# Kernel optimization log

Hardware: AMD Instinct MI355X
Metric: run time of the kernel (lower is better)

Reference implementation:

```python
import jax, jax.numpy as jnp
import numpy as np


def conv1d(x, w, b):
    # x: (N, Cin, W), w: (Cout, Cin, K) -> (N, Cout, W-K+1), VALID conv (torch Conv1d)
    y = jax.lax.conv_general_dilated(x, w, (1,), 'VALID', dimension_numbers=('NCH', 'OIH', 'NCH'))
    return y + b[None, :, None]


def cnn_block(x, w, b):
    # conv1d then MaxPool1d over the full valid length -> (N, Cout)
    return jnp.max(conv1d(x, w, b), axis=2)


def highway(x, Wp, bp, Wg, bg):
    p = jax.nn.relu(x @ Wp.T + bp)
    g = jax.nn.sigmoid(x @ Wg.T + bg)
    return g * p + (1.0 - g) * x


def lstm_masked(x, lens, Wih, Whh, bih, bhh):
    # x: (N, Wt, E); lens: (N,) valid lengths. Emulates pack_padded_sequence +
    # nn.LSTM + pad_packed_sequence: outputs are h_t for t < len, zeros after.
    N, Wt, _ = x.shape
    H = Whh.shape[1]
    bias = bih + bhh
    h0 = jnp.zeros((N, H), x.dtype)

    def step(carry, inp):
        xt, t = inp
        h, c = carry
        z = xt @ Wih.T + h @ Whh.T + bias  # (N, 4H), gate order i,f,g,o
        i, f, g, o = jnp.split(z, 4, axis=-1)
        c2 = jax.nn.sigmoid(f) * c + jax.nn.sigmoid(i) * jnp.tanh(g)
        h2 = jax.nn.sigmoid(o) * jnp.tanh(c2)
        valid = (t < lens)[:, None]
        h2 = jnp.where(valid, h2, h)
        c2 = jnp.where(valid, c2, c)
        return (h2, c2), jnp.where(valid, h2, jnp.zeros_like(h2))

    xs = jnp.moveaxis(x, 1, 0)  # (Wt, N, E)
    ts = jnp.arange(Wt)
    _, out = jax.lax.scan(step, (h0, h0), (xs, ts))
    return jnp.moveaxis(out, 0, 1)  # (N, Wt, H)


def setup_inputs() -> dict:
    key = jax.random.key(0)
    ks = jax.random.split(key, 32)
    B, T = 32, 48
    WL, WA, WE = 33, 50, 30
    EL, EA, EE, H = 300, 988, 20, 128
    CL, CA, CE = 128, 256, 64
    s = 0.02
    inp = {
        'x_lin': jax.random.normal(ks[0], (B, T, WL, EL), jnp.float32),
        'x_aco': jax.random.normal(ks[1], (B, T, WA, EA), jnp.float32),
        'x_emo': jax.random.normal(ks[2], (B, T, WE, EE), jnp.float32),
        'window_length': jax.random.randint(ks[3], (B, T), 0, WE).astype(jnp.int32) + 1,
        'length': jax.random.randint(ks[4], (B,), 1, T + 1).astype(jnp.int32),
        # CNN params
        'convL_w': s * jax.random.normal(ks[5], (CL, EL, 5), jnp.float32),
        'convL_b': jnp.zeros((CL,), jnp.float32),
        'convA_w': s * jax.random.normal(ks[6], (CA, EA, 10), jnp.float32),
        'convA_b': jnp.zeros((CA,), jnp.float32),
        'convE_w': s * jax.random.normal(ks[7], (CE, H, 3), jnp.float32),
        'convE_b': jnp.zeros((CE,), jnp.float32),
        # Highway params
        'hwL_Wp': s * jax.random.normal(ks[8], (CL, CL), jnp.float32),
        'hwL_bp': jnp.zeros((CL,), jnp.float32),
        'hwL_Wg': s * jax.random.normal(ks[9], (CL, CL), jnp.float32),
        'hwL_bg': jnp.zeros((CL,), jnp.float32),
        'hwA_Wp': s * jax.random.normal(ks[10], (CA, CA), jnp.float32),
        'hwA_bp': jnp.zeros((CA,), jnp.float32),
        'hwA_Wg': s * jax.random.normal(ks[11], (CA, CA), jnp.float32),
        'hwA_bg': jnp.zeros((CA,), jnp.float32),
        'hwE_Wp': s * jax.random.normal(ks[12], (CE, CE), jnp.float32),
        'hwE_bp': jnp.zeros((CE,), jnp.float32),
        'hwE_Wg': s * jax.random.normal(ks[13], (CE, CE), jnp.float32),
        'hwE_bg': jnp.zeros((CE,), jnp.float32),
        # LSTM params (nn.LSTM, 1 layer, batch_first)
        'lstm_Wih': s * jax.random.normal(ks[14], (4 * H, EE), jnp.float32),
        'lstm_Whh': s * jax.random.normal(ks[15], (4 * H, H), jnp.float32),
        'lstm_bih': jnp.zeros((4 * H,), jnp.float32),
        'lstm_bhh': jnp.zeros((4 * H,), jnp.float32),
    }
    return inp


def reference(x_lin, x_aco, x_emo, window_length, length,
              convL_w, convL_b, convA_w, convA_b, convE_w, convE_b,
              hwL_Wp, hwL_bp, hwL_Wg, hwL_bg,
              hwA_Wp, hwA_bp, hwA_Wg, hwA_bg,
              hwE_Wp, hwE_bp, hwE_Wg, hwE_bg,
              lstm_Wih, lstm_Whh, lstm_bih, lstm_bhh):
    B, T = x_lin.shape[:2]
    # Linguistic: per-window CNN + Highway (dropout = identity in eval)
    xl = x_lin.reshape(B * T, x_lin.shape[2], x_lin.shape[3]).transpose(0, 2, 1)  # (BT, 300, WL)
    outL = highway(cnn_block(xl, convL_w, convL_b), hwL_Wp, hwL_bp, hwL_Wg, hwL_bg)
    outL = outL.reshape(B, T, -1)
    # Acoustic
    xa = x_aco.reshape(B * T, x_aco.shape[2], x_aco.shape[3]).transpose(0, 2, 1)  # (BT, 988, WA)
    outA = highway(cnn_block(xa, convA_w, convA_b), hwA_Wp, hwA_bp, hwA_Wg, hwA_bg)
    outA = outA.reshape(B, T, -1)
    # Emotient: ragged per-window LSTM (packed semantics) -> CNN -> Highway
    xe = x_emo.reshape(B * T, x_emo.shape[2], x_emo.shape[3])  # (BT, WE, 20)
    lens = window_length.reshape(B * T)
    h = lstm_masked(xe, lens, lstm_Wih, lstm_Whh, lstm_bih, lstm_bhh)  # (BT, WE, 128)
    outE = highway(cnn_block(h.transpose(0, 2, 1), convE_w, convE_b), hwE_Wp, hwE_bp, hwE_Wg, hwE_bg)
    outE = outE.reshape(B, T, -1)
    # Concatenate modalities -> (B, T, 128+256+64) fed to the downstream head
    return jnp.concatenate([outL, outA, outE], axis=2)
```

## Files before the change

kernel.cpp:

```cpp
#include <hip/hip_runtime.h>
#include <hip/hip_bf16.h>
#include <math.h>

#define BTOT 1536
#define EL 300
#define ELP 304
#define WL_ 33
#define CL 128
#define LOUTL 29
#define KPL 1536
#define EA 988
#define EAP 992
#define WA_ 50
#define CA 256
#define LOUTA 41
#define KPA 9920
#define EE 20
#define WE_ 30
#define HH 128
#define CE 64
#define LOUTE 28
#define KPE 384
#define KDIML 1500
#define KDIMA 9880
#define KDIME 384

typedef __attribute__((ext_vector_type(4))) float f32x4;
typedef __attribute__((ext_vector_type(8))) short short8;

__device__ __forceinline__ unsigned short f2bf(float f) {
    unsigned int x = __float_as_uint(f);
    unsigned int r = (x + 0x7fffu + ((x >> 16) & 1u)) >> 16;
    return (unsigned short)r;
}

__device__ __forceinline__ float sigmf(float x) {
    return __builtin_amdgcn_rcpf(1.f + __expf(-x));
}
__device__ __forceinline__ float tanh_fast(float x) {
    return 1.f - 2.f * __builtin_amdgcn_rcpf(1.f + __expf(2.f * x));
}

#define GLD16(gp, lp) __builtin_amdgcn_global_load_lds( \
    (const __attribute__((address_space(1))) void*)(gp), \
    (__attribute__((address_space(3))) void*)(lp), 16, 0, 0)

template<int N> __device__ __forceinline__ void vmwait() {
    if constexpr (N == 0) asm volatile("s_waitcnt vmcnt(0)" ::: "memory");
    else if constexpr (N == 2) asm volatile("s_waitcnt vmcnt(2)" ::: "memory");
    else if constexpr (N == 3) asm volatile("s_waitcnt vmcnt(3)" ::: "memory");
    else static_assert(N == 0 || N == 2 || N == 3, "add case");
}

__device__ __forceinline__ void tr_one(const float* a, float* at, int R, int C, int idx) {
    int r = idx / C, c = idx - r * C;
    at[c * R + r] = a[idx];
}
template<int CIN, int CINP, int KW, int COUT, int KPAD>
__device__ __forceinline__ void wt_one(const float* w, unsigned short* wt, int idx) {
    int co = idx / KPAD;
    int p  = idx - co * KPAD;
    int k  = p / CINP;
    int c  = p - k * CINP;
    float v = 0.f;
    if (k < KW && c < CIN) v = w[(co * CIN + c) * KW + k];
    wt[idx] = f2bf(v);
}
template<bool BIG>
__global__ void prep_small(const float* hwL_Wp, float* WpTL, const float* hwL_Wg, float* WgTL,
                           const float* hwA_Wp, float* WpTA, const float* hwA_Wg, float* WgTA,
                           const float* hwE_Wp, float* WpTE, const float* hwE_Wg, float* WgTE,
                           const float* lstm_Wih, float* WihT, const float* lstm_Whh, float* WhhT,
                           const float* convL_w, unsigned short* wtL,
                           const float* convE_w, unsigned short* wtE,
                           unsigned short* whh_bf, unsigned short* wihp_bf) {
    constexpr int S1 = 16384, S2 = 16384, S3 = 65536, S4 = 65536, S5 = 4096, S6 = 4096;
    constexpr int S7 = 512 * 20, S8 = 512 * 128;
    constexpr int S9 = 128 * KPL, S10 = 64 * KPE, S11 = 512 * 128, S12 = 512 * 32;
    constexpr int SMALL = S1 + S2 + S3 + S4 + S5 + S6 + S7 + S8;
    constexpr int TOTAL = BIG ? (SMALL + S9 + S10 + S11 + S12) : SMALL;
    int stride = gridDim.x * blockDim.x;
    for (int i = blockIdx.x * blockDim.x + threadIdx.x; i < TOTAL; i += stride) {
        int idx = i;
        if (idx < S1) { tr_one(hwL_Wp, WpTL, 128, 128, idx); continue; } idx -= S1;
        if (idx < S2) { tr_one(hwL_Wg, WgTL, 128, 128, idx); continue; } idx -= S2;
        if (idx < S3) { tr_one(hwA_Wp, WpTA, 256, 256, idx); continue; } idx -= S3;
        if (idx < S4) { tr_one(hwA_Wg, WgTA, 256, 256, idx); continue; } idx -= S4;
        if (idx < S5) { tr_one(hwE_Wp, WpTE, 64, 64, idx); continue; } idx -= S5;
        if (idx < S6) { tr_one(hwE_Wg, WgTE, 64, 64, idx); continue; } idx -= S6;
        if (idx < S7) { tr_one(lstm_Wih, WihT, 512, 20, idx); continue; } idx -= S7;
        if (idx < S8) { tr_one(lstm_Whh, WhhT, 512, 128, idx); continue; } idx -= S8;
        if constexpr (BIG) {
            if (idx < S9) { wt_one<EL, ELP, 5, CL, KPL>(convL_w, wtL, idx); continue; } idx -= S9;
            if (idx < S10) { wt_one<HH, HH, 3, CE, KPE>(convE_w, wtE, idx); continue; } idx -= S10;
            if (idx < S11) { whh_bf[idx] = f2bf(lstm_Whh[idx]); continue; } idx -= S11;
            { int col = idx >> 5, e = idx & 31;
              wihp_bf[idx] = (e < 20) ? f2bf(lstm_Wih[col * 20 + e]) : (unsigned short)0; }
        }
    }
}

__global__ void prep_wtA(const float* __restrict__ w, unsigned short* __restrict__ wt) {
    int idx = blockIdx.x * blockDim.x + threadIdx.x;
    if (idx >= CA * KPA) return;
    wt_one<EA, EAP, 10, CA, KPA>(w, wt, idx);
}

template<int CIN, int CINP>
__device__ __forceinline__ void cvt_chunk(const float* in, unsigned short* out, int idx) {
    constexpr int CH = CINP / 8;
    int row = idx / CH, c0 = (idx - row * CH) * 8;
    const float* src = in + (size_t)row * CIN + c0;
    union { short8 s; unsigned short u[8]; } o;
    if (c0 + 8 <= CIN) {
        float4 v0 = *(const float4*)src;
        float4 v1 = *(const float4*)(src + 4);
        o.u[0]=f2bf(v0.x); o.u[1]=f2bf(v0.y); o.u[2]=f2bf(v0.z); o.u[3]=f2bf(v0.w);
        o.u[4]=f2bf(v1.x); o.u[5]=f2bf(v1.y); o.u[6]=f2bf(v1.z); o.u[7]=f2bf(v1.w);
    } else {
        #pragma unroll
        for (int j = 0; j < 8; ++j) o.u[j] = (c0 + j < CIN) ? f2bf(src[j]) : (unsigned short)0;
    }
    *(short8*)(out + (size_t)row * CINP + c0) = o.s;
}
__global__ void cvt_both(const float* __restrict__ xa, const float* __restrict__ xl,
                         unsigned short* __restrict__ outa, unsigned short* __restrict__ outl) {
    constexpr int NAC = (BTOT * WA_) * (EAP / 8);
    constexpr int NLC = (BTOT * WL_) * (ELP / 8);
    int stride = gridDim.x * blockDim.x;
    for (int i = blockIdx.x * blockDim.x + threadIdx.x; i < NAC + NLC; i += stride) {
        if (i < NAC) cvt_chunk<EA, EAP>(xa, outa, i);
        else         cvt_chunk<EL, ELP>(xl, outl, i - NAC);
    }
}

template<int NBT, int LOUT, int WIN, int CINP, int COUT, int KPAD>
__global__ __launch_bounds__(512, 4)
void conv_pool_v5(const unsigned short* __restrict__ xb, const unsigned short* __restrict__ wt,
                  const float* __restrict__ bias, float* __restrict__ pooled)
{
    constexpr int NF   = COUT / 64;
    constexpr int NK   = KPAD / 32;
    constexpr int NBU  = COUT / 16;
    constexpr int BWI  = (NBU > 8) ? NBU / 8 : 1;
    constexpr int VMN  = 1 + BWI;
    constexpr int ABY  = 128 * 64;
    constexpr int BUFB = ABY + COUT * 64;
    constexpr int MVAL = NBT * LOUT;

    __shared__ __align__(16) char smem[3 * BUFB > 32768 ? 3 * BUFB : 32768];

    const int tid  = threadIdx.x;
    const int lane = tid & 63;
    const int wid  = tid >> 6;
    const int wm   = wid >> 2;
    const int wn   = wid & 3;
    const int lr   = lane & 15;
    const int lq   = lane >> 4;
    const int bx   = blockIdx.x;

    f32x4 acc[4][NF];
    #pragma unroll
    for (int i = 0; i < 4; ++i)
        #pragma unroll
        for (int j = 0; j < NF; ++j) acc[i][j] = (f32x4){0.f, 0.f, 0.f, 0.f};

    const int sr   = wid * 16 + (lane >> 2);
    const int sslt = lane & 3;
    int rv = (sr < MVAL) ? sr : (MVAL - 1);
    int sbtl = rv / LOUT;
    int sl   = rv - sbtl * LOUT;
    const char* asrc0 = (const char*)xb + (((size_t)(bx * NBT + sbtl) * WIN + sl) * CINP) * 2
                      + ((sslt * 16) ^ (((sr >> 2) & 3) << 4));

    auto STAGE = [&](int ts, int buf) {
        char* db = smem + buf * BUFB;
        GLD16(asrc0 + (size_t)ts * 64, db + wid * 1024 + lane * 16);
        #pragma unroll
        for (int i = 0; i < BWI; ++i) {
            int bu = (NBU > 8) ? (wid + i * 8) : (wid & (NBU - 1));
            int col = bu * 16 + (lane >> 2);
            const char* src = (const char*)wt + (size_t)col * KPAD * 2
                + (size_t)ts * 64 + ((sslt * 16) ^ (((col >> 2) & 3) << 4));
            GLD16(src, db + ABY + bu * 1024 + lane * 16);
        }
    };

    STAGE(0, 0);
    STAGE(1, 1);
    vmwait<VMN>();
    __builtin_amdgcn_s_barrier();

    const int ra = wm * 64 + lr;
    int cur = 0;
    for (int t = 0; t < NK; ++t) {
        const char* sA = smem + cur * BUFB;
        const char* sB = sA + ABY;
        short8 a[4];
        #pragma unroll
        for (int o = 0; o < 4; ++o) {
            int r = ra + o * 16;
            a[o] = *(const short8*)(sA + (size_t)r * 64 + ((lq * 16) ^ (((r >> 2) & 3) << 4)));
        }
        short8 bfr[NF];
        #pragma unroll
        for (int nf = 0; nf < NF; ++nf) {
            int cb = wn * (16 * NF) + nf * 16 + lr;
            bfr[nf] = *(const short8*)(sB + (size_t)cb * 64 + ((lq * 16) ^ (((cb >> 2) & 3) << 4)));
        }
        int wb = cur + 2; if (wb >= 3) wb -= 3;
        if (t + 2 < NK) STAGE(t + 2, wb);
        asm volatile("s_waitcnt lgkmcnt(0)" ::: "memory");
        __builtin_amdgcn_sched_barrier(0);
        __builtin_amdgcn_s_setprio(1);
        #pragma unroll
        for (int nf = 0; nf < NF; ++nf)
            #pragma unroll
            for (int o = 0; o < 4; ++o)
                acc[o][nf] = __builtin_amdgcn_mfma_f32_16x16x32_bf16(a[o], bfr[nf], acc[o][nf], 0, 0, 0);
        __builtin_amdgcn_s_setprio(0);
        if (t + 2 < NK) vmwait<VMN>(); else vmwait<0>();
        asm volatile("" ::: "memory");
        __builtin_amdgcn_s_barrier();
        cur = cur + 1; if (cur >= 3) cur -= 3;
    }
    __syncthreads();

    for (int nf = 0; nf < NF; ++nf) {
        #pragma unroll
        for (int m = 0; m < 4; ++m) {
            int row = wm * 64 + m * 16 + lq * 4;
            int cs  = wn * 16 + lr;
            f32x4 v = acc[m][nf];
            #pragma unroll
            for (int r = 0; r < 4; ++r)
                *(float*)(smem + (size_t)(row + r) * 256 + ((cs * 4) ^ (((row + r) & 7) << 4))) = v[r];
        }
        __syncthreads();
        if (tid < 64 * NBT) {
            int btl = tid >> 6, cs = tid & 63;
            int base = btl * LOUT;
            float m = *(const float*)(smem + (size_t)base * 256 + ((cs * 4) ^ ((base & 7) << 4)));
            for (int l = 1; l < LOUT; ++l) {
                int rr = base + l;
                m = fmaxf(m, *(const float*)(smem + (size_t)rr * 256 + ((cs * 4) ^ ((rr & 7) << 4))));
            }
            int col = (cs >> 4) * (16 * NF) + nf * 16 + (cs & 15);
            int bt  = bx * NBT + btl;
            pooled[(size_t)bt * COUT + col] = m + bias[col];
        }
        __syncthreads();
    }
}

__global__ __launch_bounds__(512, 1)
void lstm_mfma(const float* __restrict__ x_emo,
               const unsigned short* __restrict__ wihp_bf, const unsigned short* __restrict__ whh_bf,
               const float* __restrict__ bih, const float* __restrict__ bhh,
               const int* __restrict__ lens, unsigned short* __restrict__ hbuf)
{
    __shared__ __align__(16) unsigned short xq[WE_ * 16 * 32];
    __shared__ __align__(16) char h_s[2 * 16 * HH * 2];

    const int tid  = threadIdx.x;
    const int w    = tid >> 6;
    const int lane = tid & 63;
    const int lr   = lane & 15;
    const int lq   = lane >> 4;
    const int s0   = blockIdx.x * 16;
    const int c    = w * 16 + lr;

    short8 bfr[4][4];
    short8 bw[4];
    float bj[4];
    #pragma unroll
    for (int g = 0; g < 4; ++g) {
        int col = g * 128 + c;
        #pragma unroll
        for (int kt = 0; kt < 4; ++kt)
            bfr[g][kt] = *(const short8*)(whh_bf + (size_t)col * 128 + kt * 32 + lq * 8);
        bw[g] = *(const short8*)(wihp_bf + (size_t)col * 32 + lq * 8);
        bj[g] = bih[col] + bhh[col];
    }
    int len4[4];
    #pragma unroll
    for (int j = 0; j < 4; ++j) len4[j] = lens[s0 + lq * 4 + j];

    for (int i = tid; i < WE_ * 16 * 32; i += 512) {
        int t = i >> 9, r = (i >> 5) & 15, e = i & 31;
        xq[i] = (e < 20) ? f2bf(x_emo[(((size_t)(s0 + r) * WE_) + t) * 20 + e]) : (unsigned short)0;
    }
    for (int i = tid; i < 2048; i += 512) ((unsigned int*)h_s)[i] = 0u;

    float c_prev[4] = {0.f, 0.f, 0.f, 0.f};
    unsigned short hb_prev[4] = {0, 0, 0, 0};
    __syncthreads();

    for (int t = 0; t < WE_; ++t) {
        const char* hsr = h_s + (t & 1) * 4096;
        char* hsw = h_s + ((t & 1) ^ 1) * 4096;
        short8 ax = *(const short8*)((const char*)xq + (size_t)(t * 16 + lr) * 64 + lq * 16);
        short8 af[4];
        #pragma unroll
        for (int kt = 0; kt < 4; ++kt)
            af[kt] = *(const short8*)(hsr + ((lr * 256 + kt * 64 + lq * 16) ^ ((lr & 7) << 4)));
        f32x4 acc[4];
        #pragma unroll
        for (int g = 0; g < 4; ++g)
            acc[g] = __builtin_amdgcn_mfma_f32_16x16x32_bf16(ax, bw[g], (f32x4){0.f,0.f,0.f,0.f}, 0, 0, 0);
        #pragma unroll
        for (int kt = 0; kt < 4; ++kt)
            #pragma unroll
            for (int g = 0; g < 4; ++g)
                acc[g] = __builtin_amdgcn_mfma_f32_16x16x32_bf16(af[kt], bfr[g][kt], acc[g], 0, 0, 0);
        #pragma unroll
        for (int j = 0; j < 4; ++j) {
            int s = lq * 4 + j;
            float zi = acc[0][j] + bj[0];
            float zf = acc[1][j] + bj[1];
            float zg = acc[2][j] + bj[2];
            float zo = acc[3][j] + bj[3];
            float si = sigmf(zi), sf = sigmf(zf), so = sigmf(zo);
            float tg = tanh_fast(zg);
            float c2 = sf * c_prev[j] + si * tg;
            float h2 = so * tanh_fast(c2);
            bool valid = (t < len4[j]);
            c_prev[j] = valid ? c2 : c_prev[j];
            unsigned short h2b = f2bf(h2);
            unsigned short hn = valid ? h2b : hb_prev[j];
            hb_prev[j] = hn;
            *(unsigned short*)(hsw + (((s * HH + c) * 2) ^ ((s & 7) << 4))) = hn;
            hbuf[(((size_t)(s0 + s) * WE_) + t) * HH + c] = valid ? h2b : (unsigned short)0;
        }
        __syncthreads();
    }
}

template<int C, int OFF>
__global__ void highway_kernel(const float* __restrict__ pooled,
                               const float* __restrict__ WpT, const float* __restrict__ bp,
                               const float* __restrict__ WgT, const float* __restrict__ bg,
                               float* __restrict__ out) {
    int bt = blockIdx.x;
    int j  = threadIdx.x;
    __shared__ float xs[C];
    xs[j] = pooled[(size_t)bt * C + j];
    __syncthreads();
    float ap = bp[j], ag = bg[j];
    for (int cc = 0; cc < C; ++cc) {
        float xv = xs[cc];
        ap += xv * WpT[cc * C + j];
        ag += xv * WgT[cc * C + j];
    }
    float p = fmaxf(ap, 0.f);
    float g = sigmf(ag);
    out[(size_t)bt * 448 + OFF + j] = g * p + (1.f - g) * xs[j];
}

__global__ __launch_bounds__(512)
void lstm_kernel_f32(const float* __restrict__ x, const int* __restrict__ lens,
                     const float* __restrict__ WihT, const float* __restrict__ WhhT,
                     const float* __restrict__ bih, const float* __restrict__ bhh,
                     float* __restrict__ hout) {
    int bt = blockIdx.x;
    int j  = threadIdx.x;
    __shared__ float xs[WE_][EE];
    __shared__ __align__(16) float hs[HH];
    __shared__ float zs[512];
    for (int idx = j; idx < WE_ * EE; idx += 512)
        ((float*)xs)[idx] = x[(size_t)bt * WE_ * EE + idx];
    if (j < HH) hs[j] = 0.f;
    float wih[EE];
    #pragma unroll
    for (int e = 0; e < EE; ++e) wih[e] = WihT[e * 512 + j];
    float whh[HH];
    #pragma unroll
    for (int h = 0; h < HH; ++h) whh[h] = WhhT[h * 512 + j];
    float bjv = bih[j] + bhh[j];
    float c_reg = 0.f;
    int len = lens[bt];
    __syncthreads();
    for (int t = 0; t < WE_; ++t) {
        float z = bjv;
        #pragma unroll
        for (int e = 0; e < EE; ++e) z += wih[e] * xs[t][e];
        const float4* h4 = (const float4*)hs;
        #pragma unroll
        for (int q = 0; q < HH / 4; ++q) {
            float4 hv = h4[q];
            z += whh[4*q+0] * hv.x + whh[4*q+1] * hv.y
               + whh[4*q+2] * hv.z + whh[4*q+3] * hv.w;
        }
        zs[j] = z;
        __syncthreads();
        if (j < HH) {
            float zi = zs[j], zf = zs[HH + j], zg = zs[2*HH + j], zo = zs[3*HH + j];
            float si = 1.f / (1.f + expf(-zi));
            float sf = 1.f / (1.f + expf(-zf));
            float so = 1.f / (1.f + expf(-zo));
            float tg = tanhf(zg);
            float c2 = sf * c_reg + si * tg;
            float h2 = so * tanhf(c2);
            bool valid = (t < len);
            float hn = valid ? h2 : hs[j];
            c_reg    = valid ? c2 : c_reg;
            hout[((size_t)bt * WE_ + t) * HH + j] = valid ? h2 : 0.f;
            hs[j] = hn;
        }
        __syncthreads();
    }
}

template<int CIN, int WIN, int COUT, int KDIM, int LOUT>
__global__ __launch_bounds__(256)
void conv_pool_simple(const float* __restrict__ x, const float* __restrict__ w,
                      const float* __restrict__ bias, float* __restrict__ pooled)
{
    constexpr int KW = KDIM / CIN;
    int bt = blockIdx.x;
    int co = blockIdx.y * 64 + (threadIdx.x & 63);
    int seg = threadIdx.x >> 6;
    __shared__ float part[4][64];
    float m = -INFINITY;
    for (int l = seg; l < LOUT; l += 4) {
        float acc = 0.f;
        for (int k = 0; k < KW; ++k) {
            const float* xr = x + ((size_t)bt * WIN + l + k) * CIN;
            const float* wr = w + ((size_t)co * CIN) * KW + k;
            for (int cc = 0; cc < CIN; ++cc) acc += xr[cc] * wr[(size_t)cc * KW];
        }
        m = fmaxf(m, acc);
    }
    part[seg][threadIdx.x & 63] = m;
    __syncthreads();
    if (threadIdx.x < 64) {
        float mm = fmaxf(fmaxf(part[0][threadIdx.x], part[1][threadIdx.x]),
                         fmaxf(part[2][threadIdx.x], part[3][threadIdx.x]));
        pooled[(size_t)bt * COUT + co] = mm + bias[co];
    }
}

static inline int cdiv(int a, int b) { return (a + b - 1) / b; }

extern "C" void kernel_launch(void* const* d_in, const int* in_sizes, int n_in,
                              void* d_out, int out_size, void* d_ws, size_t ws_size,
                              hipStream_t stream) {
    const float* x_lin  = (const float*)d_in[0];
    const float* x_aco  = (const float*)d_in[1];
    const float* x_emo  = (const float*)d_in[2];
    const int*   wlen   = (const int*)  d_in[3];
    const float* convL_w = (const float*)d_in[5];
    const float* convL_b = (const float*)d_in[6];
    const float* convA_w = (const float*)d_in[7];
    const float* convA_b = (const float*)d_in[8];
    const float* convE_w = (const float*)d_in[9];
    const float* convE_b = (const float*)d_in[10];
    const float* hwL_Wp = (const float*)d_in[11];
    const float* hwL_bp = (const float*)d_in[12];
    const float* hwL_Wg = (const float*)d_in[13];
    const float* hwL_bg = (const float*)d_in[14];
    const float* hwA_Wp = (const float*)d_in[15];
    const float* hwA_bp = (const float*)d_in[16];
    const float* hwA_Wg = (const float*)d_in[17];
    const float* hwA_bg = (const float*)d_in[18];
    const float* hwE_Wp = (const float*)d_in[19];
    const float* hwE_bp = (const float*)d_in[20];
    const float* hwE_Wg = (const float*)d_in[21];
    const float* hwE_bg = (const float*)d_in[22];
    const float* lstm_Wih = (const float*)d_in[23];
    const float* lstm_Whh = (const float*)d_in[24];
    const float* lstm_bih = (const float*)d_in[25];
    const float* lstm_bhh = (const float*)d_in[26];
    float* out = (float*)d_out;

    char* p0 = (char*)d_ws;
    char* p = p0;
    auto alloc = [&](size_t bytes) { char* r = p; p += (bytes + 255) & ~(size_t)255; return r; };
    float* WpTL = (float*)alloc((size_t)CL * CL * 4);
    float* WgTL = (float*)alloc((size_t)CL * CL * 4);
    float* WpTA = (float*)alloc((size_t)CA * CA * 4);
    float* WgTA = (float*)alloc((size_t)CA * CA * 4);
    float* WpTE = (float*)alloc((size_t)CE * CE * 4);
    float* WgTE = (float*)alloc((size_t)CE * CE * 4);
    float* WihT = (float*)alloc((size_t)EE * 512 * 4);
    float* WhhT = (float*)alloc((size_t)HH * 512 * 4);
    unsigned short* whh_bf  = (unsigned short*)alloc((size_t)512 * 128 * 2);
    unsigned short* wihp_bf = (unsigned short*)alloc((size_t)512 * 32 * 2);
    void*  hbuf = (void*)alloc((size_t)BTOT * WE_ * HH * 4);
    float* pL   = (float*)alloc((size_t)BTOT * CL * 4);
    float* pA   = (float*)alloc((size_t)BTOT * CA * 4);
    float* pE   = (float*)alloc((size_t)BTOT * CE * 4);
    unsigned short* wtA = (unsigned short*)alloc((size_t)CA * KPA * 2);
    unsigned short* wtL = (unsigned short*)alloc((size_t)CL * KPL * 2);
    unsigned short* wtE = (unsigned short*)alloc((size_t)CE * KPE * 2);
    unsigned short* xlin_p = (unsigned short*)alloc((size_t)BTOT * WL_ * ELP * 2 + 64);
    unsigned short* xaco_p = (unsigned short*)alloc((size_t)BTOT * WA_ * EAP * 2 + 64);
    size_t need = (size_t)(p - p0);
    bool big = ws_size >= need;

    if (big) {
        prep_small<true><<<2048, 256, 0, stream>>>(hwL_Wp, WpTL, hwL_Wg, WgTL, hwA_Wp, WpTA, hwA_Wg, WgTA,
                                                   hwE_Wp, WpTE, hwE_Wg, WgTE, lstm_Wih, WihT, lstm_Whh, WhhT,
                                                   convL_w, wtL, convE_w, wtE, whh_bf, wihp_bf);
        prep_wtA<<<cdiv(CA * KPA, 256), 256, 0, stream>>>(convA_w, wtA);
        lstm_mfma<<<BTOT / 16, 512, 0, stream>>>(x_emo, wihp_bf, whh_bf, lstm_bih, lstm_bhh, wlen,
                                                 (unsigned short*)hbuf);
        cvt_both<<<4096, 256, 0, stream>>>(x_aco, x_lin, xaco_p, xlin_p);
        conv_pool_v5<3, LOUTA, WA_, EAP, CA, KPA>
            <<<BTOT / 3, 512, 0, stream>>>(xaco_p, wtA, convA_b, pA);
        conv_pool_v5<4, LOUTL, WL_, ELP, CL, KPL>
            <<<BTOT / 4, 512, 0, stream>>>(xlin_p, wtL, convL_b, pL);
        conv_pool_v5<4, LOUTE, WE_, HH, CE, KPE>
            <<<BTOT / 4, 512, 0, stream>>>((const unsigned short*)hbuf, wtE, convE_b, pE);
    } else {
        prep_small<false><<<2048, 256, 0, stream>>>(hwL_Wp, WpTL, hwL_Wg, WgTL, hwA_Wp, WpTA, hwA_Wg, WgTA,
                                                    hwE_Wp, WpTE, hwE_Wg, WgTE, lstm_Wih, WihT, lstm_Whh, WhhT,
                                                    convL_w, wtL, convE_w, wtE, whh_bf, wihp_bf);
        lstm_kernel_f32<<<BTOT, 512, 0, stream>>>(x_emo, wlen, WihT, WhhT, lstm_bih, lstm_bhh, (float*)hbuf);
        conv_pool_simple<EA, WA_, CA, KDIMA, LOUTA>
            <<<dim3(BTOT, CA / 64), 256, 0, stream>>>(x_aco, convA_w, convA_b, pA);
        conv_pool_simple<EL, WL_, CL, KDIML, LOUTL>
            <<<dim3(BTOT, CL / 64), 256, 0, stream>>>(x_lin, convL_w, convL_b, pL);
        conv_pool_simple<HH, WE_, CE, KDIME, LOUTE>
            <<<dim3(BTOT, CE / 64), 256, 0, stream>>>((const float*)hbuf, convE_w, convE_b, pE);
    }

    highway_kernel<CL, 0>  <<<BTOT, CL, 0, stream>>>(pL, WpTL, hwL_bp, WgTL, hwL_bg, out);
    highway_kernel<CA, 128><<<BTOT, CA, 0, stream>>>(pA, WpTA, hwA_bp, WgTA, hwA_bg, out);
    highway_kernel<CE, 384><<<BTOT, CE, 0, stream>>>(pE, WpTE, hwE_bp, WgTE, hwE_bg, out);
}
```

Measured before the change: 613.3 us.

## Retile conv-pool GEMM into 256-thread blocks with N-split and fuse highway launches

The conv+maxpool implicit GEMM kernel is rewritten with templated BM/BN tiles and 256-thread blocks at two blocks per CU. For the acoustic branch, each block now covers 6 windows (M=256) and half the output channels (N=128), with an XCD-aware block-to-tile mapping. The LDS swizzle and the pooling epilogue are adjusted to match, using a padded row stride. The three highway launches are merged into one kernel to cut launch overhead, at the cost of some idle threads in the L/E blocks and different register pressure and occupancy in the GEMM.

```diff
diff --git a/kernel.cpp b/kernel.cpp
--- a/kernel.cpp
+++ b/kernel.cpp
@@ -47,9 +47,10 @@
 
 template<int N> __device__ __forceinline__ void vmwait() {
     if constexpr (N == 0) asm volatile("s_waitcnt vmcnt(0)" ::: "memory");
-    else if constexpr (N == 2) asm volatile("s_waitcnt vmcnt(2)" ::: "memory");
     else if constexpr (N == 3) asm volatile("s_waitcnt vmcnt(3)" ::: "memory");
-    else static_assert(N == 0 || N == 2 || N == 3, "add case");
+    else if constexpr (N == 4) asm volatile("s_waitcnt vmcnt(4)" ::: "memory");
+    else if constexpr (N == 6) asm volatile("s_waitcnt vmcnt(6)" ::: "memory");
+    else static_assert(N == 0 || N == 3 || N == 4 || N == 6, "add case");
 }
 
 __device__ __forceinline__ void tr_one(const float* a, float* at, int R, int C, int idx) {
@@ -134,56 +135,76 @@
     }
 }
 
-template<int NBT, int LOUT, int WIN, int CINP, int COUT, int KPAD>
-__global__ __launch_bounds__(512, 4)
-void conv_pool_v5(const unsigned short* __restrict__ xb, const unsigned short* __restrict__ wt,
+template<int NBT, int LOUT, int WIN, int CINP, int COUT, int KPAD, int BM, int BN, int NS>
+__global__ __launch_bounds__(256, 2)
+void conv_pool_v6(const unsigned short* __restrict__ xb, const unsigned short* __restrict__ wt,
                   const float* __restrict__ bias, float* __restrict__ pooled)
 {
-    constexpr int NF   = COUT / 64;
+    constexpr int MFR  = BM / 32;
+    constexpr int NFR  = BN / 32;
+    constexpr int A_IT = BM / 64;
+    constexpr int B_IT = BN / 64;
+    constexpr int VMN  = A_IT + B_IT;
+    constexpr int ABY  = BM * 64;
+    constexpr int BUFB = (BM + BN) * 64;
     constexpr int NK   = KPAD / 32;
-    constexpr int NBU  = COUT / 16;
-    constexpr int BWI  = (NBU > 8) ? NBU / 8 : 1;
-    constexpr int VMN  = 1 + BWI;
-    constexpr int ABY  = 128 * 64;
-    constexpr int BUFB = ABY + COUT * 64;
     constexpr int MVAL = NBT * LOUT;
-
-    __shared__ __align__(16) char smem[3 * BUFB > 32768 ? 3 * BUFB : 32768];
+    constexpr int MT   = BTOT / NBT;
+    constexpr int EPI  = BM * 36 * 4;
+    constexpr int SMSZ = (3 * BUFB > EPI) ? 3 * BUFB : EPI;
+
+    __shared__ __align__(16) char smem[SMSZ];
 
     const int tid  = threadIdx.x;
     const int lane = tid & 63;
     const int wid  = tid >> 6;
-    const int wm   = wid >> 2;
-    const int wn   = wid & 3;
+    const int wm   = wid >> 1;
+    const int wn   = wid & 1;
     const int lr   = lane & 15;
     const int lq   = lane >> 4;
-    const int bx   = blockIdx.x;
-
-    f32x4 acc[4][NF];
-    #pragma unroll
-    for (int i = 0; i < 4; ++i)
-        #pragma unroll
-        for (int j = 0; j < NF; ++j) acc[i][j] = (f32x4){0.f, 0.f, 0.f, 0.f};
-
-    const int sr   = wid * 16 + (lane >> 2);
-    const int sslt = lane & 3;
-    int rv = (sr < MVAL) ? sr : (MVAL - 1);
-    int sbtl = rv / LOUT;
-    int sl   = rv - sbtl * LOUT;
-    const char* asrc0 = (const char*)xb + (((size_t)(bx * NBT + sbtl) * WIN + sl) * CINP) * 2
-                      + ((sslt * 16) ^ (((sr >> 2) & 3) << 4));
+
+    int m, n;
+    if constexpr (NS == 2) {
+        int xcd = blockIdx.x & 7;
+        n = xcd & 1;
+        m = (xcd >> 1) * (MT / 4) + (blockIdx.x >> 3);
+    } else {
+        m = blockIdx.x; n = 0;
+    }
+
+    f32x4 acc[MFR][NFR];
+    #pragma unroll
+    for (int i = 0; i < MFR; ++i)
+        #pragma unroll
+        for (int j = 0; j < NFR; ++j) acc[i][j] = (f32x4){0.f, 0.f, 0.f, 0.f};
+
+    const char* asrc[A_IT];
+    #pragma unroll
+    for (int i = 0; i < A_IT; ++i) {
+        int c = tid + i * 256;
+        int r = c >> 2, slot = c & 3;
+        int rv = (r < MVAL) ? r : (MVAL - 1);
+        int btl = rv / LOUT, l = rv - btl * LOUT;
+        asrc[i] = (const char*)xb + (((size_t)(m * NBT + btl) * WIN + l) * CINP) * 2
+                + ((slot * 16) ^ (((r >> 1) & 3) << 4));
+    }
+    const char* bsrc[B_IT];
+    #pragma unroll
+    for (int i = 0; i < B_IT; ++i) {
+        int c = tid + i * 256;
+        int col = c >> 2, slot = c & 3;
+        bsrc[i] = (const char*)wt + ((size_t)(n * BN + col) * KPAD) * 2
+                + ((slot * 16) ^ (((col >> 1) & 3) << 4));
+    }
 
     auto STAGE = [&](int ts, int buf) {
         char* db = smem + buf * BUFB;
-        GLD16(asrc0 + (size_t)ts * 64, db + wid * 1024 + lane * 16);
-        #pragma unroll
-        for (int i = 0; i < BWI; ++i) {
-            int bu = (NBU > 8) ? (wid + i * 8) : (wid & (NBU - 1));
-            int col = bu * 16 + (lane >> 2);
-            const char* src = (const char*)wt + (size_t)col * KPAD * 2
-                + (size_t)ts * 64 + ((sslt * 16) ^ (((col >> 2) & 3) << 4));
-            GLD16(src, db + ABY + bu * 1024 + lane * 16);
-        }
+        #pragma unroll
+        for (int i = 0; i < A_IT; ++i)
+            GLD16(asrc[i] + (size_t)ts * 64, db + i * 4096 + wid * 1024);
+        #pragma unroll
+        for (int i = 0; i < B_IT; ++i)
+            GLD16(bsrc[i] + (size_t)ts * 64, db + ABY + i * 4096 + wid * 1024);
     };
 
     STAGE(0, 0);
@@ -191,22 +212,23 @@
     vmwait<VMN>();
     __builtin_amdgcn_s_barrier();
 
-    const int ra = wm * 64 + lr;
+    const int rbase = wm * (BM / 2) + lr;
+    const int cbase = wn * (BN / 2) + lr;
     int cur = 0;
     for (int t = 0; t < NK; ++t) {
         const char* sA = smem + cur * BUFB;
         const char* sB = sA + ABY;
-        short8 a[4];
-        #pragma unroll
-        for (int o = 0; o < 4; ++o) {
-            int r = ra + o * 16;
-            a[o] = *(const short8*)(sA + (size_t)r * 64 + ((lq * 16) ^ (((r >> 2) & 3) << 4)));
-        }
-        short8 bfr[NF];
-        #pragma unroll
-        for (int nf = 0; nf < NF; ++nf) {
-            int cb = wn * (16 * NF) + nf * 16 + lr;
-            bfr[nf] = *(const short8*)(sB + (size_t)cb * 64 + ((lq * 16) ^ (((cb >> 2) & 3) << 4)));
+        short8 a[MFR];
+        #pragma unroll
+        for (int o = 0; o < MFR; ++o) {
+            int r = rbase + o * 16;
+            a[o] = *(const short8*)(sA + (size_t)r * 64 + ((lq * 16) ^ (((r >> 1) & 3) << 4)));
+        }
+        short8 bfr[NFR];
+        #pragma unroll
+        for (int nf = 0; nf < NFR; ++nf) {
+            int cb = cbase + nf * 16;
+            bfr[nf] = *(const short8*)(sB + (size_t)cb * 64 + ((lq * 16) ^ (((cb >> 1) & 3) << 4)));
         }
         int wb = cur + 2; if (wb >= 3) wb -= 3;
         if (t + 2 < NK) STAGE(t + 2, wb);
@@ -214,9 +236,9 @@
         __builtin_amdgcn_sched_barrier(0);
         __builtin_amdgcn_s_setprio(1);
         #pragma unroll
-        for (int nf = 0; nf < NF; ++nf)
+        for (int nf = 0; nf < NFR; ++nf)
             #pragma unroll
-            for (int o = 0; o < 4; ++o)
+            for (int o = 0; o < MFR; ++o)
                 acc[o][nf] = __builtin_amdgcn_mfma_f32_16x16x32_bf16(a[o], bfr[nf], acc[o][nf], 0, 0, 0);
         __builtin_amdgcn_s_setprio(0);
         if (t + 2 < NK) vmwait<VMN>(); else vmwait<0>();
@@ -226,28 +248,27 @@
     }
     __syncthreads();
 
-    for (int nf = 0; nf < NF; ++nf) {
-        #pragma unroll
-        for (int m = 0; m < 4; ++m) {
-            int row = wm * 64 + m * 16 + lq * 4;
+    float* smf = (float*)smem;
+    for (int nf = 0; nf < NFR; ++nf) {
+        #pragma unroll
+        for (int o = 0; o < MFR; ++o) {
+            int row = wm * (BM / 2) + o * 16 + lq * 4;
             int cs  = wn * 16 + lr;
-            f32x4 v = acc[m][nf];
+            f32x4 v = acc[o][nf];
             #pragma unroll
             for (int r = 0; r < 4; ++r)
-                *(float*)(smem + (size_t)(row + r) * 256 + ((cs * 4) ^ (((row + r) & 7) << 4))) = v[r];
-        }
-        __syncthreads();
-        if (tid < 64 * NBT) {
-            int btl = tid >> 6, cs = tid & 63;
+                smf[(size_t)(row + r) * 36 + cs] = v[r];
+        }
+        __syncthreads();
+        if (tid < 32 * NBT) {
+            int btl = tid >> 5, cs = tid & 31;
             int base = btl * LOUT;
-            float m = *(const float*)(smem + (size_t)base * 256 + ((cs * 4) ^ ((base & 7) << 4)));
-            for (int l = 1; l < LOUT; ++l) {
-                int rr = base + l;
-                m = fmaxf(m, *(const float*)(smem + (size_t)rr * 256 + ((cs * 4) ^ ((rr & 7) << 4))));
-            }
-            int col = (cs >> 4) * (16 * NF) + nf * 16 + (cs & 15);
-            int bt  = bx * NBT + btl;
-            pooled[(size_t)bt * COUT + col] = m + bias[col];
+            float mx = smf[(size_t)base * 36 + cs];
+            for (int l = 1; l < LOUT; ++l)
+                mx = fmaxf(mx, smf[(size_t)(base + l) * 36 + cs]);
+            int col = n * BN + (cs >> 4) * (BN / 2) + nf * 16 + (cs & 15);
+            int bt  = m * NBT + btl;
+            pooled[(size_t)bt * COUT + col] = mx + bias[col];
         }
         __syncthreads();
     }
@@ -336,25 +357,58 @@
     }
 }
 
-template<int C, int OFF>
-__global__ void highway_kernel(const float* __restrict__ pooled,
-                               const float* __restrict__ WpT, const float* __restrict__ bp,
-                               const float* __restrict__ WgT, const float* __restrict__ bg,
-                               float* __restrict__ out) {
-    int bt = blockIdx.x;
-    int j  = threadIdx.x;
-    __shared__ float xs[C];
-    xs[j] = pooled[(size_t)bt * C + j];
-    __syncthreads();
-    float ap = bp[j], ag = bg[j];
-    for (int cc = 0; cc < C; ++cc) {
-        float xv = xs[cc];
-        ap += xv * WpT[cc * C + j];
-        ag += xv * WgT[cc * C + j];
-    }
-    float p = fmaxf(ap, 0.f);
-    float g = sigmf(ag);
-    out[(size_t)bt * 448 + OFF + j] = g * p + (1.f - g) * xs[j];
+__global__ __launch_bounds__(256)
+void highway_all(const float* __restrict__ pL, const float* __restrict__ pA, const float* __restrict__ pE,
+                 const float* __restrict__ WpTL, const float* __restrict__ bpL,
+                 const float* __restrict__ WgTL, const float* __restrict__ bgL,
+                 const float* __restrict__ WpTA, const float* __restrict__ bpA,
+                 const float* __restrict__ WgTA, const float* __restrict__ bgA,
+                 const float* __restrict__ WpTE, const float* __restrict__ bpE,
+                 const float* __restrict__ WgTE, const float* __restrict__ bgE,
+                 float* __restrict__ out) {
+    __shared__ float xs[256];
+    int bx = blockIdx.x;
+    int tid = threadIdx.x;
+    if (bx < BTOT) {
+        xs[tid] = pA[(size_t)bx * 256 + tid];
+        __syncthreads();
+        float ap = bpA[tid], ag = bgA[tid];
+        for (int c = 0; c < 256; ++c) {
+            float xv = xs[c];
+            ap += xv * WpTA[c * 256 + tid];
+            ag += xv * WgTA[c * 256 + tid];
+        }
+        float pp = fmaxf(ap, 0.f);
+        float g = sigmf(ag);
+        out[(size_t)bx * 448 + 128 + tid] = g * pp + (1.f - g) * xs[tid];
+    } else {
+        int bt = bx - BTOT;
+        if (tid < 128) xs[tid] = pL[(size_t)bt * 128 + tid];
+        else if (tid < 192) xs[64 + tid] = pE[(size_t)bt * 64 + (tid - 128)];
+        __syncthreads();
+        if (tid < 128) {
+            float ap = bpL[tid], ag = bgL[tid];
+            for (int c = 0; c < 128; ++c) {
+                float xv = xs[c];
+                ap += xv * WpTL[c * 128 + tid];
+                ag += xv * WgTL[c * 128 + tid];
+            }
+            float pp = fmaxf(ap, 0.f);
+            float g = sigmf(ag);
+            out[(size_t)bt * 448 + tid] = g * pp + (1.f - g) * xs[tid];
+        } else if (tid < 192) {
+            int j = tid - 128;
+            float ap = bpE[j], ag = bgE[j];
+            for (int c = 0; c < 64; ++c) {
+                float xv = xs[192 + c];
+                ap += xv * WpTE[c * 64 + j];
+                ag += xv * WgTE[c * 64 + j];
+            }
+            float pp = fmaxf(ap, 0.f);
+            float g = sigmf(ag);
+            out[(size_t)bt * 448 + 384 + j] = g * pp + (1.f - g) * xs[192 + j];
+        }
+    }
 }
 
 __global__ __launch_bounds__(512)
@@ -506,12 +560,12 @@
         lstm_mfma<<<BTOT / 16, 512, 0, stream>>>(x_emo, wihp_bf, whh_bf, lstm_bih, lstm_bhh, wlen,
                                                  (unsigned short*)hbuf);
         cvt_both<<<4096, 256, 0, stream>>>(x_aco, x_lin, xaco_p, xlin_p);
-        conv_pool_v5<3, LOUTA, WA_, EAP, CA, KPA>
-            <<<BTOT / 3, 512, 0, stream>>>(xaco_p, wtA, convA_b, pA);
-        conv_pool_v5<4, LOUTL, WL_, ELP, CL, KPL>
-            <<<BTOT / 4, 512, 0, stream>>>(xlin_p, wtL, convL_b, pL);
-        conv_pool_v5<4, LOUTE, WE_, HH, CE, KPE>
-            <<<BTOT / 4, 512, 0, stream>>>((const unsigned short*)hbuf, wtE, convE_b, pE);
+        conv_pool_v6<6, LOUTA, WA_, EAP, CA, KPA, 256, 128, 2>
+            <<<512, 256, 0, stream>>>(xaco_p, wtA, convA_b, pA);
+        conv_pool_v6<4, LOUTL, WL_, ELP, CL, KPL, 128, 128, 1>
+            <<<BTOT / 4, 256, 0, stream>>>(xlin_p, wtL, convL_b, pL);
+        conv_pool_v6<4, LOUTE, WE_, HH, CE, KPE, 128, 64, 1>
+            <<<BTOT / 4, 256, 0, stream>>>((const unsigned short*)hbuf, wtE, convE_b, pE);
     } else {
         prep_small<false><<<2048, 256, 0, stream>>>(hwL_Wp, WpTL, hwL_Wg, WgTL, hwA_Wp, WpTA, hwA_Wg, WgTA,
                                                     hwE_Wp, WpTE, hwE_Wg, WgTE, lstm_Wih, WihT, lstm_Whh, WhhT,
@@ -525,7 +579,8 @@
             <<<dim3(BTOT, CE / 64), 256, 0, stream>>>((const float*)hbuf, convE_w, convE_b, pE);
     }
 
-    highway_kernel<CL, 0>  <<<BTOT, CL, 0, stream>>>(pL, WpTL, hwL_bp, WgTL, hwL_bg, out);
-    highway_kernel<CA, 128><<<BTOT, CA, 0, stream>>>(pA, WpTA, hwA_bp, WgTA, hwA_bg, out);
-    highway_kernel<CE, 384><<<BTOT, CE, 0, stream>>>(pE, WpTE, hwE_bp, WgTE, hwE_bg, out);
-}
+    highway_all<<<2 * BTOT, 256, 0, stream>>>(pL, pA, pE,
+                                              WpTL, hwL_bp, WgTL, hwL_bg,
+                                              WpTA, hwA_bp, WgTA, hwA_bg,
+                                              WpTE, hwE_bp, WgTE, hwE_bg, out);
+}
```

Measured after the change: 627.4 us. 2.3% more time.
